# Kernel optimization log

Measured on AMD Instinct MI355X. Metric: run time of the kernel, lower is better.

The kernel has to match this reference:

```python
import jax, jax.numpy as jnp
import numpy as np

B, L, D, T = 32, 512, 1024, 256
MAX_MENTION_LEN = 10
NEG_INF = float('-inf')


def _static_bounds_and_keep():
    # Full (start, end) grid, flattened row-major like torch's .view(-1, 2)
    s = np.repeat(np.arange(L), L)
    e = np.tile(np.arange(L), L)
    bounds = np.stack([s, e], axis=-1)            # [L*L, 2]
    keep = (e - s) <= MAX_MENTION_LEN             # static per-position mask
    idx = np.nonzero(keep)[0]
    return jnp.asarray(bounds[keep], jnp.int32), jnp.asarray(idx, jnp.int32)


def setup_inputs() -> dict:
    key = jax.random.key(0)
    k0, k1, k2 = jax.random.split(key, 3)
    text_encodings = jax.random.normal(k0, (B, L, D), dtype=jnp.float32)
    mask_ctxt = jnp.ones((B, L), dtype=jnp.int32)
    # word -> wordpiece mapping: [start, end_exclusive); values kept in [1, L)
    tokens_mapping = jax.random.randint(k1, (B, T, 2), 1, L).astype(jnp.int32)
    W = jax.random.normal(k2, (D, 3), dtype=jnp.float32) * 0.02
    b = jnp.zeros((3,), dtype=jnp.float32)
    return {"text_encodings": text_encodings, "mask_ctxt": mask_ctxt,
            "tokens_mapping": tokens_mapping, "W": W, "b": b}


def reference(text_encodings, mask_ctxt, tokens_mapping, W, b):
    # per-token start / end / mention logits
    logits = jnp.einsum('bld,dk->blk', text_encodings, W) + b  # [B, L, 3]
    valid_tok = (mask_ctxt == 1)
    start_lp = jnp.where(valid_tok, logits[:, :, 0], NEG_INF)
    end_lp = jnp.where(valid_tok, logits[:, :, 1], NEG_INF)
    mention_lp = jnp.where(valid_tok, logits[:, :, 2], NEG_INF)

    # scores[b, s, e] = start[b, s] + end[b, e] + sum_{i=s..e} mention[b, i]
    scores = start_lp[:, :, None] + end_lp[:, None, :]          # [B, L, L]
    csum = jnp.cumsum(mention_lp, axis=1)                        # [B, L]
    csum_prev = jnp.concatenate(
        [jnp.zeros((csum.shape[0], 1), csum.dtype), csum[:, :-1]], axis=1)
    scores = scores + (csum[:, None, :] - csum_prev[:, :, None])

    # mention_sizes > 0  <=>  e >= s
    pos = jnp.arange(L)
    size_ok = pos[None, :, None] <= pos[None, None, :]           # [1, L, L]

    # token-boundary masks (scatter 1 at word starts / ends, zero col 0)
    bidx = jnp.arange(tokens_mapping.shape[0])[:, None]
    ts = jnp.zeros(mask_ctxt.shape, jnp.int32).at[bidx, tokens_mapping[:, :, 0]].set(1)
    ts = ts.at[:, 0].set(0)
    te = jnp.zeros(mask_ctxt.shape, jnp.int32).at[bidx, tokens_mapping[:, :, 1] - 1].set(1)
    te = te.at[:, 0].set(0)
    vse = ts[:, :, None] * te[:, None, :]                        # bmm outer product

    valid = size_ok & (mask_ctxt[:, :, None] > 0) & (vse > 0)
    scores = jnp.where(valid, scores, NEG_INF)

    scores_flat = scores.reshape(scores.shape[0], -1)            # [B, L*L]
    bounds_keep, keep_idx = _static_bounds_and_keep()
    out_scores = scores_flat[:, keep_idx]                        # [B, K]
    out_bounds = jnp.broadcast_to(bounds_keep[None],
                                  (scores.shape[0],) + bounds_keep.shape)
    return out_scores, out_bounds
```

## Files before the change

### kernel.cpp

```cpp
#include <hip/hip_runtime.h>
#include <math.h>

#define BB 32
#define LL 512
#define DD 1024
#define TT 256
#define NK 136393
#define NK_LIN 131273
#define S_LIN 502
#define NEG_BIG  -3.0e38f
#define NEG_MASK -1.0e30f
#define P_TOT (BB * NK)
#define SC4 (P_TOT / 4)
#define GEMV_BLOCKS (BB * LL / 4)
#define TAIL_CNT (BB * 11)
#define MEMSET_CNT ((SC4 + 255) / 256)
#define BCHUNKS ((NK + 255) / 256)
#define D2_BLOCKS (TAIL_CNT + MEMSET_CNT + 2 * BCHUNKS)

typedef float f4v __attribute__((ext_vector_type(4)));
typedef float f2v __attribute__((ext_vector_type(2)));

__device__ __forceinline__ int off_s(int s) {
    return (s <= S_LIN) ? s * (s + 21) / 2 : NK_LIN + (s - S_LIN) * LL;
}
__device__ __forceinline__ void invert(int k, int& s, int& e) {
    if (k >= NK_LIN) {
        const int r = k - NK_LIN;
        s = S_LIN + (r >> 9);
        e = r & 511;
    } else {
        float f = sqrtf(8.0f * (float)k + 441.0f);
        s = (int)((f - 21.0f) * 0.5f);
        if (s < 0) s = 0;
        if (s > 501) s = 501;
        while ((s + 1) * (s + 22) / 2 <= k) ++s;
        while (s * (s + 21) / 2 > k) --s;
        e = k - s * (s + 21) / 2;
    }
}

__global__ __launch_bounds__(256) void gemv_kernel(
    const float* __restrict__ text, const float* __restrict__ W,
    const float* __restrict__ bias, const int* __restrict__ mask,
    float* __restrict__ slp, float* __restrict__ elp, float* __restrict__ mlp)
{
    const int wid  = threadIdx.x >> 6;
    const int lane = threadIdx.x & 63;
    const int row  = blockIdx.x * 4 + wid;
    const f4v* t4 = (const f4v*)(text + (size_t)row * DD);
    const f4v* w4 = (const f4v*)W;
    float a0 = 0.f, a1 = 0.f, a2 = 0.f;
#pragma unroll
    for (int j = 0; j < 4; ++j) {
        const int fi = lane + j * 64;
        f4v v  = t4[fi];
        f4v w0 = w4[fi * 3 + 0];
        f4v w1 = w4[fi * 3 + 1];
        f4v w2 = w4[fi * 3 + 2];
        a0 += v.x * w0.x;  a1 += v.x * w0.y;  a2 += v.x * w0.z;
        a0 += v.y * w0.w;  a1 += v.y * w1.x;  a2 += v.y * w1.y;
        a0 += v.z * w1.z;  a1 += v.z * w1.w;  a2 += v.z * w2.x;
        a0 += v.w * w2.y;  a1 += v.w * w2.z;  a2 += v.w * w2.w;
    }
#pragma unroll
    for (int o = 32; o; o >>= 1) {
        a0 += __shfl_down(a0, o);
        a1 += __shfl_down(a1, o);
        a2 += __shfl_down(a2, o);
    }
    if (lane == 0) {
        const int m = mask[row];
        slp[row] = (m == 1) ? a0 + bias[0] : NEG_MASK;
        elp[row] = (m == 1) ? a1 + bias[1] : NEG_MASK;
        mlp[row] = (m == 1) ? a2 + bias[2] : NEG_MASK;
    }
}

__global__ __launch_bounds__(256) void emit_kernel(
    const float* __restrict__ slp, const float* __restrict__ elp,
    const float* __restrict__ mlp, const int* __restrict__ tmap,
    float* __restrict__ out)
{
    const int id = blockIdx.x;
    const int t  = threadIdx.x;

    if (id < TAIL_CNT) {
        const int b = id / 11;
        const int j = id - b * 11;
        __shared__ float sl[LL], el[LL], ml[LL];
        __shared__ unsigned char tsl[LL], tel[LL];
        const int base = b * LL;
#pragma unroll
        for (int h = 0; h < 2; ++h) {
            const int i = t + h * 256;
            sl[i] = slp[base + i]; el[i] = elp[base + i]; ml[i] = mlp[base + i];
            tsl[i] = 0; tel[i] = 0;
        }
        __syncthreads();
        if (t < TT) {
            int s0 = tmap[((size_t)b * TT + t) * 2 + 0];
            int e0 = tmap[((size_t)b * TT + t) * 2 + 1] - 1;
            s0 = min(max(s0, 0), LL - 1);
            e0 = min(max(e0, 0), LL - 1);
            tsl[s0] = 1;
            tel[e0] = 1;
        }
        __syncthreads();
#pragma unroll
        for (int h = 0; h < 2; ++h) {
            const int s = t + h * 256;
            const int e = s + j;
            if (e < LL) {
                float v = NEG_BIG;
                if (s > 0 && tsl[s] && tel[e]) {
                    float w = 0.f;
                    for (int l = s; l <= e; ++l) w += ml[l];
                    v = sl[s] + el[e] + w;
                    if (v < -1.0e29f) v = NEG_BIG;
                }
                out[(size_t)b * NK + off_s(s) + e] = v;
            }
        }
        return;
    }

    if (id < TAIL_CNT + MEMSET_CNT) {
        const int gid = (id - TAIL_CNT) * 256 + t;
        if (gid >= SC4) return;
        const int p4 = gid * 4;
        const int b  = p4 / NK;
        const int k  = p4 - b * NK;
        int s, e;
        invert(k, s, e);
        if (e + 3 < s) {
            f4v neg = {NEG_BIG, NEG_BIG, NEG_BIG, NEG_BIG};
            *(f4v*)(out + p4) = neg;
        } else {
            int rowlen = (s <= S_LIN) ? (s + 11) : LL;
#pragma unroll
            for (int kk = 0; kk < 4; ++kk) {
                if (e < s) out[p4 + kk] = NEG_BIG;
                ++e;
                if (e >= rowlen) {
                    e = 0; ++s;
                    if (s >= LL) s = 0;
                    rowlen = (s <= S_LIN) ? (s + 11) : LL;
                }
            }
        }
        return;
    }

    const int q = id - TAIL_CNT - MEMSET_CNT;
    const int g = (q >= BCHUNKS) ? 1 : 0;
    const int c = q - g * BCHUNKS;
    const int p = c * 256 + t;
    if (p >= NK) return;
    int s, e;
    invert(p, s, e);
    f2v v = {(float)s, (float)e};
    f2v* bp = (f2v*)(out + (size_t)P_TOT);
#pragma unroll
    for (int j = 0; j < 16; ++j) {
        const int b = g * 16 + j;
        bp[(size_t)b * NK + p] = v;
    }
}

extern "C" void kernel_launch(void* const* d_in, const int* in_sizes, int n_in,
                              void* d_out, int out_size, void* d_ws, size_t ws_size,
                              hipStream_t stream) {
    const float* text = (const float*)d_in[0];
    const int*   mask = (const int*)d_in[1];
    const int*   tmap = (const int*)d_in[2];
    const float* W    = (const float*)d_in[3];
    const float* bias = (const float*)d_in[4];
    float* out = (float*)d_out;

    float* slp = (float*)d_ws;
    float* elp = slp + (size_t)BB * LL;
    float* mlp = elp + (size_t)BB * LL;

    gemv_kernel<<<GEMV_BLOCKS, 256, 0, stream>>>(text, W, bias, mask,
                                                 slp, elp, mlp);
    emit_kernel<<<D2_BLOCKS, 256, 0, stream>>>(slp, elp, mlp, tmap, out);
}
```

Measured before the change: 27.72 us.

## Move token-boundary flags into GEMV kernel and emit scores via vectorized fill

Token-boundary start/end flags are now computed per batch in extra blocks of the first kernel and written to workspace. The second kernel drops the separate per-diagonal tail blocks. Each fill thread computes all four scores of its float4 chunk directly, reading flags and logits from global memory, and writes one vector store. This removes the scattered scalar writes and the duplicate tmap scatter. In exchange, valid entries now do uncached global loads for the mention prefix loop instead of using shared memory.

```diff
diff --git a/kernel.cpp b/kernel.cpp
--- a/kernel.cpp
+++ b/kernel.cpp
@@ -13,10 +13,10 @@
 #define P_TOT (BB * NK)
 #define SC4 (P_TOT / 4)
 #define GEMV_BLOCKS (BB * LL / 4)
-#define TAIL_CNT (BB * 11)
-#define MEMSET_CNT ((SC4 + 255) / 256)
+#define D1_BLOCKS (GEMV_BLOCKS + BB)
+#define ROWFILL_CNT ((SC4 + 255) / 256)
 #define BCHUNKS ((NK + 255) / 256)
-#define D2_BLOCKS (TAIL_CNT + MEMSET_CNT + 2 * BCHUNKS)
+#define D2_BLOCKS (ROWFILL_CNT + 2 * BCHUNKS)
 
 typedef float f4v __attribute__((ext_vector_type(4)));
 typedef float f2v __attribute__((ext_vector_type(2)));
@@ -43,11 +43,41 @@
 __global__ __launch_bounds__(256) void gemv_kernel(
     const float* __restrict__ text, const float* __restrict__ W,
     const float* __restrict__ bias, const int* __restrict__ mask,
-    float* __restrict__ slp, float* __restrict__ elp, float* __restrict__ mlp)
+    const int* __restrict__ tmap,
+    float* __restrict__ slp, float* __restrict__ elp, float* __restrict__ mlp,
+    int* __restrict__ fs, int* __restrict__ fe)
 {
-    const int wid  = threadIdx.x >> 6;
-    const int lane = threadIdx.x & 63;
-    const int row  = blockIdx.x * 4 + wid;
+    const int id = blockIdx.x;
+    const int t  = threadIdx.x;
+
+    if (id >= GEMV_BLOCKS) {
+        const int b = id - GEMV_BLOCKS;
+        __shared__ unsigned char tsl[LL], tel[LL];
+        tsl[t] = 0; tsl[t + 256] = 0;
+        tel[t] = 0; tel[t + 256] = 0;
+        __syncthreads();
+        {
+            int s0 = tmap[((size_t)b * TT + t) * 2 + 0];
+            int e0 = tmap[((size_t)b * TT + t) * 2 + 1] - 1;
+            s0 = min(max(s0, 0), LL - 1);
+            e0 = min(max(e0, 0), LL - 1);
+            tsl[s0] = 1;
+            tel[e0] = 1;
+        }
+        __syncthreads();
+#pragma unroll
+        for (int h = 0; h < 2; ++h) {
+            const int l = t + h * 256;
+            const int idx = b * LL + l;
+            fs[idx] = (l != 0 && tsl[l] && mask[idx] == 1) ? 1 : 0;
+            fe[idx] = (l != 0 && tel[l]) ? 1 : 0;
+        }
+        return;
+    }
+
+    const int wid  = t >> 6;
+    const int lane = t & 63;
+    const int row  = id * 4 + wid;
     const f4v* t4 = (const f4v*)(text + (size_t)row * DD);
     const f4v* w4 = (const f4v*)W;
     float a0 = 0.f, a1 = 0.f, a2 = 0.f;
@@ -77,82 +107,57 @@
     }
 }
 
-__global__ __launch_bounds__(256) void emit_kernel(
+__global__ __launch_bounds__(256) void fill_kernel(
     const float* __restrict__ slp, const float* __restrict__ elp,
-    const float* __restrict__ mlp, const int* __restrict__ tmap,
-    float* __restrict__ out)
+    const float* __restrict__ mlp, const int* __restrict__ fs,
+    const int* __restrict__ fe, float* __restrict__ out)
 {
     const int id = blockIdx.x;
     const int t  = threadIdx.x;
 
-    if (id < TAIL_CNT) {
-        const int b = id / 11;
-        const int j = id - b * 11;
-        __shared__ float sl[LL], el[LL], ml[LL];
-        __shared__ unsigned char tsl[LL], tel[LL];
-        const int base = b * LL;
+    if (id < ROWFILL_CNT) {
+        const int gid = id * 256 + t;
+        if (gid >= SC4) return;
+        const int p4 = gid * 4;
+        int b = p4 / NK;
+        int k = p4 - b * NK;
+        int s, e;
+        invert(k, s, e);
+
+        if (e + 3 < s) {
+            f4v neg = {NEG_BIG, NEG_BIG, NEG_BIG, NEG_BIG};
+            *(f4v*)(out + p4) = neg;
+            return;
+        }
+
+        float vals[4];
+        int rowlen = (s <= S_LIN) ? (s + 11) : LL;
 #pragma unroll
-        for (int h = 0; h < 2; ++h) {
-            const int i = t + h * 256;
-            sl[i] = slp[base + i]; el[i] = elp[base + i]; ml[i] = mlp[base + i];
-            tsl[i] = 0; tel[i] = 0;
-        }
-        __syncthreads();
-        if (t < TT) {
-            int s0 = tmap[((size_t)b * TT + t) * 2 + 0];
-            int e0 = tmap[((size_t)b * TT + t) * 2 + 1] - 1;
-            s0 = min(max(s0, 0), LL - 1);
-            e0 = min(max(e0, 0), LL - 1);
-            tsl[s0] = 1;
-            tel[e0] = 1;
-        }
-        __syncthreads();
-#pragma unroll
-        for (int h = 0; h < 2; ++h) {
-            const int s = t + h * 256;
-            const int e = s + j;
-            if (e < LL) {
-                float v = NEG_BIG;
-                if (s > 0 && tsl[s] && tel[e]) {
+        for (int kk = 0; kk < 4; ++kk) {
+            float v = NEG_BIG;
+            if (e >= s && s > 0) {
+                const int base = b * LL;
+                if (fs[base + s] && fe[base + e]) {
                     float w = 0.f;
-                    for (int l = s; l <= e; ++l) w += ml[l];
-                    v = sl[s] + el[e] + w;
+                    for (int l = s; l <= e; ++l) w += mlp[base + l];
+                    v = slp[base + s] + elp[base + e] + w;
                     if (v < -1.0e29f) v = NEG_BIG;
                 }
-                out[(size_t)b * NK + off_s(s) + e] = v;
+            }
+            vals[kk] = v;
+            ++e;
+            if (e >= rowlen) {
+                e = 0; ++s;
+                if (s >= LL) { s = 0; ++b; }
+                rowlen = (s <= S_LIN) ? (s + 11) : LL;
             }
         }
+        f4v vv = {vals[0], vals[1], vals[2], vals[3]};
+        *(f4v*)(out + p4) = vv;
         return;
     }
 
-    if (id < TAIL_CNT + MEMSET_CNT) {
-        const int gid = (id - TAIL_CNT) * 256 + t;
-        if (gid >= SC4) return;
-        const int p4 = gid * 4;
-        const int b  = p4 / NK;
-        const int k  = p4 - b * NK;
-        int s, e;
-        invert(k, s, e);
-        if (e + 3 < s) {
-            f4v neg = {NEG_BIG, NEG_BIG, NEG_BIG, NEG_BIG};
-            *(f4v*)(out + p4) = neg;
-        } else {
-            int rowlen = (s <= S_LIN) ? (s + 11) : LL;
-#pragma unroll
-            for (int kk = 0; kk < 4; ++kk) {
-                if (e < s) out[p4 + kk] = NEG_BIG;
-                ++e;
-                if (e >= rowlen) {
-                    e = 0; ++s;
-                    if (s >= LL) s = 0;
-                    rowlen = (s <= S_LIN) ? (s + 11) : LL;
-                }
-            }
-        }
-        return;
-    }
-
-    const int q = id - TAIL_CNT - MEMSET_CNT;
+    const int q = id - ROWFILL_CNT;
     const int g = (q >= BCHUNKS) ? 1 : 0;
     const int c = q - g * BCHUNKS;
     const int p = c * 256 + t;
@@ -181,8 +186,10 @@
     float* slp = (float*)d_ws;
     float* elp = slp + (size_t)BB * LL;
     float* mlp = elp + (size_t)BB * LL;
+    int*   fs  = (int*)(mlp + (size_t)BB * LL);
+    int*   fe  = fs + (size_t)BB * LL;
 
-    gemv_kernel<<<GEMV_BLOCKS, 256, 0, stream>>>(text, W, bias, mask,
-                                                 slp, elp, mlp);
-    emit_kernel<<<D2_BLOCKS, 256, 0, stream>>>(slp, elp, mlp, tmap, out);
+    gemv_kernel<<<D1_BLOCKS, 256, 0, stream>>>(text, W, bias, mask, tmap,
+                                               slp, elp, mlp, fs, fe);
+    fill_kernel<<<D2_BLOCKS, 256, 0, stream>>>(slp, elp, mlp, fs, fe, out);
 }
```

After: 34.30 us. 23.7% more time.

## Split emit into disjoint float4 chunks: fill chunks vs diagonal-band score chunks

Applied to the files above, without the earlier changes.

The emit kernel now assigns each aligned float4 chunk of the score output to exactly one writer. Chunks made only of below-diagonal entries get a vector fill. Chunks that contain any e>=s entry are written by the band blocks as whole float4 stores, replacing the scalar per-element writes and the overlap between the fill and band paths. The band work is regrouped into 8 blocks per batch covering 64 start rows each, and the mask is folded into the start-flag array. The chunk-ownership logic near row boundaries is more intricate and easy to get wrong.

```diff
diff --git a/kernel.cpp b/kernel.cpp
--- a/kernel.cpp
+++ b/kernel.cpp
@@ -13,10 +13,10 @@
 #define P_TOT (BB * NK)
 #define SC4 (P_TOT / 4)
 #define GEMV_BLOCKS (BB * LL / 4)
-#define TAIL_CNT (BB * 11)
+#define TAILQ_CNT (BB * 8)
 #define MEMSET_CNT ((SC4 + 255) / 256)
 #define BCHUNKS ((NK + 255) / 256)
-#define D2_BLOCKS (TAIL_CNT + MEMSET_CNT + 2 * BCHUNKS)
+#define D2_BLOCKS (TAILQ_CNT + MEMSET_CNT + 2 * BCHUNKS)
 
 typedef float f4v __attribute__((ext_vector_type(4)));
 typedef float f2v __attribute__((ext_vector_type(2)));
@@ -79,80 +79,112 @@
 
 __global__ __launch_bounds__(256) void emit_kernel(
     const float* __restrict__ slp, const float* __restrict__ elp,
-    const float* __restrict__ mlp, const int* __restrict__ tmap,
-    float* __restrict__ out)
+    const float* __restrict__ mlp, const int* __restrict__ mask,
+    const int* __restrict__ tmap, float* __restrict__ out)
 {
     const int id = blockIdx.x;
     const int t  = threadIdx.x;
 
-    if (id < TAIL_CNT) {
-        const int b = id / 11;
-        const int j = id - b * 11;
+    if (id < TAILQ_CNT) {
+        const int b  = id >> 3;
+        const int r0 = (id & 7) << 6;
         __shared__ float sl[LL], el[LL], ml[LL];
-        __shared__ unsigned char tsl[LL], tel[LL];
+        __shared__ unsigned char fsb[LL], feb[LL];
         const int base = b * LL;
-#pragma unroll
-        for (int h = 0; h < 2; ++h) {
-            const int i = t + h * 256;
-            sl[i] = slp[base + i]; el[i] = elp[base + i]; ml[i] = mlp[base + i];
-            tsl[i] = 0; tel[i] = 0;
-        }
+        const int i0 = t, i1 = t + 256;
+        const int mk0 = mask[base + i0], mk1 = mask[base + i1];
+        sl[i0] = slp[base + i0]; el[i0] = elp[base + i0]; ml[i0] = mlp[base + i0];
+        sl[i1] = slp[base + i1]; el[i1] = elp[base + i1]; ml[i1] = mlp[base + i1];
+        fsb[i0] = 0; fsb[i1] = 0; feb[i0] = 0; feb[i1] = 0;
         __syncthreads();
-        if (t < TT) {
+        {
             int s0 = tmap[((size_t)b * TT + t) * 2 + 0];
             int e0 = tmap[((size_t)b * TT + t) * 2 + 1] - 1;
             s0 = min(max(s0, 0), LL - 1);
             e0 = min(max(e0, 0), LL - 1);
-            tsl[s0] = 1;
-            tel[e0] = 1;
+            fsb[s0] = 1;
+            feb[e0] = 1;
         }
         __syncthreads();
-#pragma unroll
-        for (int h = 0; h < 2; ++h) {
-            const int s = t + h * 256;
-            const int e = s + j;
-            if (e < LL) {
+        fsb[i0] = (i0 != 0 && fsb[i0] && mk0 == 1) ? 1 : 0;
+        fsb[i1] = (fsb[i1] && mk1 == 1) ? 1 : 0;
+        feb[i0] = (i0 != 0 && feb[i0]) ? 1 : 0;
+        __syncthreads();
+
+        for (int it = t; it < 64 * 5; it += 256) {
+            const int s_loc = it / 5;
+            const int slot  = it - s_loc * 5;
+            const int s     = r0 + s_loc;
+            const int offf  = b * NK + off_s(s);
+            const int rowlen = (s <= S_LIN) ? (s + 11) : LL;
+            const int p0 = ((((offf + s) >> 2) - 1 + slot) << 2);
+            if (p0 < offf || p0 >= offf + rowlen) continue;
+            float vals[4];
+            bool nonpure = false;
+#pragma unroll
+            for (int kk = 0; kk < 4; ++kk) {
+                const int p = p0 + kk;
                 float v = NEG_BIG;
-                if (s > 0 && tsl[s] && tel[e]) {
-                    float w = 0.f;
-                    for (int l = s; l <= e; ++l) w += ml[l];
-                    v = sl[s] + el[e] + w;
-                    if (v < -1.0e29f) v = NEG_BIG;
+                int rr, er;
+                if (p < offf + rowlen) { rr = s;     er = p - offf; }
+                else                   { rr = s + 1; er = p - offf - rowlen; }
+                if (rr < LL) {
+                    if (er >= rr) {
+                        nonpure = true;
+                        if (fsb[rr] && feb[er]) {
+                            float w = 0.f;
+                            for (int l = rr; l <= er; ++l) w += ml[l];
+                            v = sl[rr] + el[er] + w;
+                            if (v < -1.0e29f) v = NEG_BIG;
+                        }
+                    }
+                } else {
+                    nonpure = true;
                 }
-                out[(size_t)b * NK + off_s(s) + e] = v;
+                vals[kk] = v;
             }
+            if (nonpure) {
+                f4v vv = {vals[0], vals[1], vals[2], vals[3]};
+                *(f4v*)(out + p0) = vv;
+            }
         }
         return;
     }
 
-    if (id < TAIL_CNT + MEMSET_CNT) {
-        const int gid = (id - TAIL_CNT) * 256 + t;
+    if (id < TAILQ_CNT + MEMSET_CNT) {
+        const int gid = (id - TAILQ_CNT) * 256 + t;
         if (gid >= SC4) return;
         const int p4 = gid * 4;
-        const int b  = p4 / NK;
-        const int k  = p4 - b * NK;
+        int b = p4 / NK;
+        int k = p4 - b * NK;
         int s, e;
         invert(k, s, e);
+        bool pure;
         if (e + 3 < s) {
+            pure = true;
+        } else {
+            pure = true;
+            int ss = s, ee = e;
+            int rowlen = (ss <= S_LIN) ? (ss + 11) : LL;
+#pragma unroll
+            for (int kk = 0; kk < 4; ++kk) {
+                if (ee >= ss) { pure = false; break; }
+                ++ee;
+                if (ee >= rowlen) {
+                    ee = 0; ++ss;
+                    if (ss >= LL) ss = 0;
+                    rowlen = (ss <= S_LIN) ? (ss + 11) : LL;
+                }
+            }
+        }
+        if (pure) {
             f4v neg = {NEG_BIG, NEG_BIG, NEG_BIG, NEG_BIG};
             *(f4v*)(out + p4) = neg;
-        } else {
-            int rowlen = (s <= S_LIN) ? (s + 11) : LL;
-#pragma unroll
-            for (int kk = 0; kk < 4; ++kk) {
-                if (e < s) out[p4 + kk] = NEG_BIG;
-                ++e;
-                if (e >= rowlen) {
-                    e = 0; ++s;
-                    if (s >= LL) s = 0;
-                    rowlen = (s <= S_LIN) ? (s + 11) : LL;
-                }
-            }
         }
         return;
     }
 
-    const int q = id - TAIL_CNT - MEMSET_CNT;
+    const int q = id - TAILQ_CNT - MEMSET_CNT;
     const int g = (q >= BCHUNKS) ? 1 : 0;
     const int c = q - g * BCHUNKS;
     const int p = c * 256 + t;
@@ -184,5 +216,5 @@
 
     gemv_kernel<<<GEMV_BLOCKS, 256, 0, stream>>>(text, W, bias, mask,
                                                  slp, elp, mlp);
-    emit_kernel<<<D2_BLOCKS, 256, 0, stream>>>(slp, elp, mlp, tmap, out);
-}
+    emit_kernel<<<D2_BLOCKS, 256, 0, stream>>>(slp, elp, mlp, mask, tmap, out);
+}
```

Measured after the change: 26.68 us. 3.7% less time.
